# Performance work log

Hardware: AMD Instinct MI355X
Metric: run time of the kernel (lower is better)

## Reference

```python
import jax, jax.numpy as jnp
from jax import lax
import numpy as np

DIM = 8          # per-head dim
BN_EPS = 1e-5
ATT_EPS = 1e-15


def setup_inputs() -> dict:
    key = jax.random.key(0)
    ks = jax.random.split(key, 6)
    B, C, H, W = 2, 512, 128, 128
    total_dim = 512                      # heads(64) * dim(8)
    c3 = 3 * total_dim                   # 1536
    x = jax.random.normal(ks[0], (B, C, H, W), dtype=jnp.float32)
    w_qkv = jax.random.normal(ks[1], (c3, C), dtype=jnp.float32) * 0.02
    w_dw = jax.random.normal(ks[2], (c3, 1, 5, 5), dtype=jnp.float32) * 0.05
    w_pw = jax.random.normal(ks[3], (c3, 8, 1, 1), dtype=jnp.float32) * 0.1
    w_proj = jax.random.normal(ks[4], (512, 2 * total_dim), dtype=jnp.float32) * 0.02
    bn_gamma = jnp.ones((512,), jnp.float32)
    bn_beta = jnp.zeros((512,), jnp.float32)
    bn_mean = jnp.zeros((512,), jnp.float32)
    bn_var = jnp.ones((512,), jnp.float32)
    return {"x": x, "w_qkv": w_qkv, "w_dw": w_dw, "w_pw": w_pw, "w_proj": w_proj,
            "bn_gamma": bn_gamma, "bn_beta": bn_beta, "bn_mean": bn_mean, "bn_var": bn_var}


def reference(x, w_qkv, w_dw, w_pw, w_proj, bn_gamma, bn_beta, bn_mean, bn_var):
    B, C, H, W = x.shape
    dn = ('NCHW', 'OIHW', 'NCHW')
    # qkv: 1x1 conv, no bias/norm/act
    qkv = jnp.einsum('bchw,oc->bohw', x, w_qkv)  # (B, 1536, H, W)
    # multi-scale aggregation: 5x5 depthwise + 1x1 grouped (groups = 3*heads = 192)
    y = lax.conv_general_dilated(qkv, w_dw, (1, 1), [(2, 2), (2, 2)],
                                 feature_group_count=w_dw.shape[0], dimension_numbers=dn)
    y = lax.conv_general_dilated(y, w_pw, (1, 1), [(0, 0), (0, 0)],
                                 feature_group_count=w_pw.shape[0] // w_pw.shape[1],
                                 dimension_numbers=dn)
    mqkv = jnp.concatenate([qkv, y], axis=1)  # (B, 3072, H, W)
    N = H * W
    mqkv = mqkv.reshape(B, -1, 3 * DIM, N)    # (B, 128 heads, 24, N)
    q = jax.nn.relu(mqkv[:, :, :DIM])          # (B, h, d, N)
    k = jax.nn.relu(mqkv[:, :, DIM:2 * DIM])   # (B, h, d, N)
    v = mqkv[:, :, 2 * DIM:]                   # (B, h, d, N)
    v = jnp.pad(v, ((0, 0), (0, 0), (0, 1), (0, 0)), constant_values=1.0)  # (B,h,d+1,N)
    vk = jnp.einsum('bhdn,bhen->bhde', v, k)   # v @ k^T : (B,h,d+1,d)
    out = jnp.einsum('bhde,bhen->bhdn', vk, q)  # (B,h,d+1,N)
    out = out[:, :, :-1] / (out[:, :, -1:] + ATT_EPS)  # (B,h,d,N)
    out = out.reshape(B, -1, H, W)             # (B, 1024, H, W)
    # proj: 1x1 conv + bn2d (inference-mode affine), no act
    out = jnp.einsum('bchw,oc->bohw', out, w_proj)
    inv = bn_gamma / jnp.sqrt(bn_var + BN_EPS)
    out = out * inv[None, :, None, None] + (bn_beta - bn_mean * inv)[None, :, None, None]
    return out
```

## Files before the change

### kernel.cpp

```cpp
#include <hip/hip_runtime.h>

typedef __bf16 bf16_t;
typedef __bf16 bf16x8 __attribute__((ext_vector_type(8)));
typedef float  f32x4  __attribute__((ext_vector_type(4)));
typedef _Float16 h16;
typedef _Float16 h16x2 __attribute__((ext_vector_type(2)));
typedef _Float16 h16x4 __attribute__((ext_vector_type(4)));
typedef _Float16 h16x8 __attribute__((ext_vector_type(8)));

#define DEVINL __device__ __forceinline__

static constexpr size_t N_PIX = 16384;
static constexpr float  FIX_TAU = 2.5e-3f;

static constexpr size_t OFF_QB  = 0;
static constexpr size_t SZ_QB   = (size_t)512 * N_PIX * 2;
static constexpr size_t OFF_QR  = OFF_QB + SZ_QB;
static constexpr size_t SZ_QR   = SZ_QB;
static constexpr size_t OFF_KV  = OFF_QR + SZ_QR;
static constexpr size_t SZ_KV   = (size_t)1024 * N_PIX * 2;
static constexpr size_t OFF_Y   = OFF_KV + SZ_KV;
static constexpr size_t SZ_Y    = (size_t)1536 * N_PIX * 2;
static constexpr size_t OFF_ATT = OFF_Y + SZ_Y;
static constexpr size_t SZ_ATT  = (size_t)N_PIX * 1024 * 2;
static constexpr size_t OFF_XT  = OFF_ATT;
static constexpr size_t OFF_XTL = OFF_ATT + (size_t)N_PIX * 512 * 2;
static constexpr size_t OFF_WALL= OFF_ATT + SZ_ATT;
static constexpr size_t SZ_WALL = (size_t)1536 * 512 * 2;
static constexpr size_t OFF_WP  = OFF_WALL + SZ_WALL;
static constexpr size_t SZ_WP   = (size_t)512 * 1024 * 2;
static constexpr size_t OFF_VK  = OFF_WP + SZ_WP;
static constexpr size_t SZ_VK   = (size_t)128 * 72 * 4;
static constexpr size_t OFF_VKP = OFF_VK + SZ_VK;
static constexpr size_t SZ_VKP  = (size_t)128 * 8 * 72 * 4;
static constexpr size_t OFF_BNA = OFF_VKP + SZ_VKP;
static constexpr size_t OFF_ZP  = OFF_BNA + 2048;
static constexpr size_t OFF_W2  = OFF_ZP + 64;
static constexpr size_t SZ_W2   = (size_t)512 * 1024 * 2;
static constexpr size_t WS_NEEDED = OFF_W2 + SZ_W2;

DEVINL void gload16(const void* g, void* l) {
  __builtin_amdgcn_global_load_lds((const __attribute__((address_space(1))) void*)g,
                                   (__attribute__((address_space(3))) void*)l, 16, 0, 0);
}

__global__ __launch_bounds__(256)
void xpose_kernel(const float* __restrict__ x, h16* __restrict__ xT, h16* __restrict__ xTl) {
  __shared__ float t[32][33];
  const int n0 = blockIdx.x * 32, c0 = blockIdx.y * 32;
  const int tx = threadIdx.x & 31, ty = threadIdx.x >> 5;
#pragma unroll
  for (int r = 0; r < 4; ++r)
    t[ty + r * 8][tx] = x[(size_t)(c0 + ty + r * 8) * N_PIX + n0 + tx];
  __syncthreads();
  const int nl = threadIdx.x >> 3, sub = threadIdx.x & 7;
  const int c8 = (sub & 3) * 8, plane = sub >> 2;
  h16x8 o;
#pragma unroll
  for (int k = 0; k < 8; ++k) {
    const float v = t[c8 + k][nl];
    if (plane == 0) {
      o[k] = (h16)v;
    } else {
      const h16 hi = (h16)v;
      o[k] = (h16)(v - (float)hi);
    }
  }
  h16* dst = plane ? xTl : xT;
  *(h16x8*)&dst[(size_t)(n0 + nl) * 512 + c0 + c8] = o;
}

static constexpr int PREP_P1 = 1536 * 512;
static constexpr int PREP_P2 = 512 * 1024;
static constexpr int PREP_TOT = PREP_P1 + PREP_P2 + 512 + 16;
__global__ __launch_bounds__(256)
void prep_kernel(const float* __restrict__ wq, const float* __restrict__ wp,
                 const float* __restrict__ gam, const float* __restrict__ bet,
                 const float* __restrict__ mu, const float* __restrict__ va,
                 h16* __restrict__ wall, bf16_t* __restrict__ wpb,
                 float* __restrict__ bna, float* __restrict__ zp) {
  const int i = blockIdx.x * 256 + threadIdx.x;
  if (i < PREP_P1) {
    const int r = i >> 9, c = i & 511;
    int o;
    if (r < 512)       o = (r >> 3) * 24 + (r & 7);
    else if (r < 1024) o = ((r - 512) >> 3) * 24 + 8 + (r & 7);
    else               o = ((r - 1024) >> 3) * 24 + 16 + (r & 7);
    wall[i] = (h16)wq[(size_t)o * 512 + c];
  } else if (i < PREP_P1 + PREP_P2) {
    const int j = i - PREP_P1;
    const int m = j >> 10;
    const float inv = gam[m] / sqrtf(va[m] + 1e-5f);
    wpb[j] = (bf16_t)(wp[j] * inv);
  } else if (i < PREP_P1 + PREP_P2 + 512) {
    const int k = i - PREP_P1 - PREP_P2;
    const float inv = gam[k] / sqrtf(va[k] + 1e-5f);
    bna[k] = bet[k] - mu[k] * inv;
  } else if (i < PREP_TOT) {
    zp[i - (PREP_P1 + PREP_P2 + 512)] = 0.f;
  }
}

__global__ __launch_bounds__(256, 4)
void gemm_qkv_kernel(const h16* __restrict__ wall, const h16* __restrict__ xT,
                     h16* __restrict__ Qb, h16* __restrict__ Qr, h16* __restrict__ KV) {
  __shared__ __align__(16) h16 As[128 * 64];
  __shared__ __align__(16) h16 Bs[128 * 64];
  const int tid = threadIdx.x, wid = tid >> 6, lane = tid & 63;
  const int fr = lane & 15, fg = lane >> 4;
  const int wm = (wid >> 1) * 64, wn = (wid & 1) * 64;
  const int by = blockIdx.y;
  const bool isQ = by < 4;
  const int m0 = (isQ ? by : by - 4) * 128;
  const int n0 = blockIdx.x * 128;
  const h16* Aptr = wall + (size_t)by * 128 * 512;
  const int srow = tid >> 3;
  const int soff = (((tid & 7) ^ (srow & 7)) * 8);

  f32x4 acc[4][4] = {};

  for (int kk = 0; kk < 512; kk += 64) {
    __syncthreads();
#pragma unroll
    for (int r = 0; r < 4; ++r) {
      gload16(Aptr + (size_t)(srow + 32 * r) * 512 + kk + soff, As + (wid * 8 + 32 * r) * 64);
      gload16(xT + (size_t)(n0 + srow + 32 * r) * 512 + kk + soff, Bs + (wid * 8 + 32 * r) * 64);
    }
    __syncthreads();
#pragma unroll
    for (int ks = 0; ks < 2; ++ks) {
      h16x8 af[4], bfr[4];
#pragma unroll
      for (int i = 0; i < 4; ++i)
        af[i]  = *(const h16x8*)&As[(wm + i * 16 + fr) * 64 + (((ks * 4 + fg) ^ (fr & 7)) * 8)];
#pragma unroll
      for (int j = 0; j < 4; ++j)
        bfr[j] = *(const h16x8*)&Bs[(wn + j * 16 + fr) * 64 + (((ks * 4 + fg) ^ (fr & 7)) * 8)];
#pragma unroll
      for (int i = 0; i < 4; ++i)
#pragma unroll
        for (int j = 0; j < 4; ++j)
          acc[i][j] = __builtin_amdgcn_mfma_f32_16x16x32_f16(af[i], bfr[j], acc[i][j], 0, 0, 0);
    }
  }

#pragma unroll
  for (int i = 0; i < 4; ++i)
#pragma unroll
    for (int r = 0; r < 4; ++r) {
      const int m = m0 + wm + i * 16 + fg * 4 + r;
#pragma unroll
      for (int j = 0; j < 4; ++j) {
        const int n = n0 + wn + j * 16 + fr;
        const float v = acc[i][j][r];
        if (isQ) {
          Qb[(size_t)m * N_PIX + n] = (h16)v;
          Qr[(size_t)m * N_PIX + n] = (h16)fmaxf(0.f, v);
        } else {
          KV[(size_t)m * N_PIX + n] = (h16)v;
        }
      }
    }
}

__global__ __launch_bounds__(256)
void fix_kernel(const float* __restrict__ wq, const h16* __restrict__ xT,
                const h16* __restrict__ xTl, h16* __restrict__ Qr) {
  const int h = blockIdx.y;
  const int n = blockIdx.x * 256 + threadIdx.x;
  const int lane = threadIdx.x & 63;
  float mx = 0.f;
#pragma unroll
  for (int e = 0; e < 8; ++e)
    mx = fmaxf(mx, (float)Qr[(size_t)(h * 8 + e) * N_PIX + n]);
  unsigned long long mask = __ballot(mx < FIX_TAU);
  const int cb = blockIdx.x * 256 + ((int)threadIdx.x & ~63);
  while (mask) {
    const int bit = __builtin_ctzll(mask);
    mask &= mask - 1;
    const int np = cb + bit;
    const int c0 = lane * 8;
    const h16x8 xh = *(const h16x8*)&xT[(size_t)np * 512 + c0];
    const h16x8 xl = *(const h16x8*)&xTl[(size_t)np * 512 + c0];
    float xs[8];
#pragma unroll
    for (int u = 0; u < 8; ++u) xs[u] = (float)xh[u] + (float)xl[u];
    float acc[8];
#pragma unroll
    for (int e = 0; e < 8; ++e) {
      const float4 w0 = *(const float4*)&wq[(size_t)(h * 24 + e) * 512 + c0];
      const float4 w1 = *(const float4*)&wq[(size_t)(h * 24 + e) * 512 + c0 + 4];
      acc[e] = w0.x * xs[0] + w0.y * xs[1] + w0.z * xs[2] + w0.w * xs[3]
             + w1.x * xs[4] + w1.y * xs[5] + w1.z * xs[6] + w1.w * xs[7];
    }
#pragma unroll
    for (int e = 0; e < 8; ++e) {
      acc[e] += __shfl_xor(acc[e], 32); acc[e] += __shfl_xor(acc[e], 16);
      acc[e] += __shfl_xor(acc[e], 8);  acc[e] += __shfl_xor(acc[e], 4);
      acc[e] += __shfl_xor(acc[e], 2);  acc[e] += __shfl_xor(acc[e], 1);
    }
    if (lane < 8) {
      float v = acc[0];
#pragma unroll
      for (int e = 1; e < 8; ++e) if (lane == e) v = acc[e];
      Qr[(size_t)(h * 8 + lane) * N_PIX + np] = (h16)fmaxf(0.f, v);
    }
  }
}

__global__ __launch_bounds__(256, 4)
void gemm_proj_kernel(const bf16_t* __restrict__ A, const bf16_t* __restrict__ B,
                      float* __restrict__ Cout, const float* __restrict__ bna) {
  __shared__ __align__(16) bf16_t As[128 * 64];
  __shared__ __align__(16) bf16_t Bs[128 * 64];
  const int tid = threadIdx.x, wid = tid >> 6, lane = tid & 63;
  const int fr = lane & 15, fg = lane >> 4;
  const int wm = (wid >> 1) * 64, wn = (wid & 1) * 64;
  const int m0 = blockIdx.y * 128, n0 = blockIdx.x * 128;
  const int srow = tid >> 3;
  const int soff = (((tid & 7) ^ (srow & 7)) * 8);
  const bf16_t* Ab = A + (size_t)m0 * 1024;
  const bf16_t* Bb = B + (size_t)n0 * 1024;

  f32x4 acc[4][4] = {};

  for (int kk = 0; kk < 1024; kk += 64) {
    __syncthreads();
#pragma unroll
    for (int r = 0; r < 4; ++r) {
      gload16(Ab + (size_t)(srow + 32 * r) * 1024 + kk + soff, As + (wid * 8 + 32 * r) * 64);
      gload16(Bb + (size_t)(srow + 32 * r) * 1024 + kk + soff, Bs + (wid * 8 + 32 * r) * 64);
    }
    __syncthreads();
#pragma unroll
    for (int ks = 0; ks < 2; ++ks) {
      bf16x8 af[4], bfr[4];
#pragma unroll
      for (int i = 0; i < 4; ++i)
        af[i]  = *(const bf16x8*)&As[(wm + i * 16 + fr) * 64 + (((ks * 4 + fg) ^ (fr & 7)) * 8)];
#pragma unroll
      for (int j = 0; j < 4; ++j)
        bfr[j] = *(const bf16x8*)&Bs[(wn + j * 16 + fr) * 64 + (((ks * 4 + fg) ^ (fr & 7)) * 8)];
#pragma unroll
      for (int i = 0; i < 4; ++i)
#pragma unroll
        for (int j = 0; j < 4; ++j)
          acc[i][j] = __builtin_amdgcn_mfma_f32_16x16x32_bf16(af[i], bfr[j], acc[i][j], 0, 0, 0);
    }
  }

#pragma unroll
  for (int i = 0; i < 4; ++i)
#pragma unroll
    for (int r = 0; r < 4; ++r) {
      const int m = m0 + wm + i * 16 + fg * 4 + r;
      const float sh = bna[m];
#pragma unroll
      for (int j = 0; j < 4; ++j)
        Cout[(size_t)m * N_PIX + n0 + wn + j * 16 + fr] = acc[i][j][r] + sh;
    }
}

__global__ __launch_bounds__(256)
void dwpw_kernel(const h16* __restrict__ Qb, const h16* __restrict__ KV,
                 const float* __restrict__ wdw, const float* __restrict__ wpw,
                 const h16* __restrict__ zp, h16* __restrict__ y) {
  const int g = blockIdx.y, t = blockIdx.x;
  const int typ = g % 3, head = g / 3;
  const int ty0 = (t >> 1) * 16, tx0 = (t & 1) * 64;
  const int tid = threadIdx.x, wid = tid >> 6, lane = tid & 63;
  __shared__ __align__(16) h16 sin_[8][20][80];
  __shared__ h16x2 swd2[8][25];
  __shared__ h16x2 swp2[8][8];
  if (tid < 200) {
    const h16 w = (h16)wdw[(g * 8 + tid / 25) * 25 + tid % 25];
    h16x2 w2; w2[0] = w; w2[1] = w;
    swd2[tid / 25][tid % 25] = w2;
  }
  if (tid < 64) {
    const h16 w = (h16)wpw[(g * 8 + (tid >> 3)) * 8 + (tid & 7)];
    h16x2 w2; w2[0] = w; w2[1] = w;
    swp2[tid >> 3][tid & 7] = w2;
  }
  const h16* plane = (typ == 0) ? (Qb + (size_t)head * 8 * N_PIX)
                                : (KV + (size_t)((typ == 2 ? 512 : 0) + head * 8) * N_PIX);
  h16* sflat = &sin_[0][0][0];
  for (int base = wid * 64; base < 1600; base += 256) {
    const int id  = base + lane;
    const int ch  = id / 200;
    const int rem = id - ch * 200;
    const int row = rem / 10;
    const int c6  = rem - row * 10;
    const int gy  = ty0 + row - 2;
    const int gx  = tx0 + c6 * 8 - 8;
    const bool ok = ((unsigned)gy < 128u) && ((unsigned)gx < 128u);
    const h16* src = ok ? (plane + (size_t)ch * N_PIX + gy * 128 + gx) : zp;
    gload16(src, sflat + (size_t)base * 8);
  }
  __syncthreads();

  const int px4 = (tid & 15) * 4, py = tid >> 4;
  h16x2 dwa[8][2];
#pragma unroll
  for (int ch = 0; ch < 8; ++ch) {
    h16x2 A0 = 0, A1 = 0;
#pragma unroll
    for (int di = 0; di < 5; ++di) {
      const uint2 w0 = *(const uint2*)&sin_[ch][py + di][px4 + 4];
      const uint2 w1 = *(const uint2*)&sin_[ch][py + di][px4 + 8];
      const uint2 w2v = *(const uint2*)&sin_[ch][py + di][px4 + 12];
      const unsigned u1 = w0.y, u2 = w1.x, u3 = w1.y, u4 = w2v.x;
      const h16x2 P2 = __builtin_bit_cast(h16x2, u1);
      const h16x2 P3 = __builtin_bit_cast(h16x2, (u2 << 16) | (u1 >> 16));
      const h16x2 P4 = __builtin_bit_cast(h16x2, u2);
      const h16x2 P5 = __builtin_bit_cast(h16x2, (u3 << 16) | (u2 >> 16));
      const h16x2 P6 = __builtin_bit_cast(h16x2, u3);
      const h16x2 P7 = __builtin_bit_cast(h16x2, (u4 << 16) | (u3 >> 16));
      const h16x2 P8 = __builtin_bit_cast(h16x2, u4);
      h16x2 wd;
      wd = swd2[ch][di * 5 + 0]; A0 += wd * P2; A1 += wd * P4;
      wd = swd2[ch][di * 5 + 1]; A0 += wd * P3; A1 += wd * P5;
      wd = swd2[ch][di * 5 + 2]; A0 += wd * P4; A1 += wd * P6;
      wd = swd2[ch][di * 5 + 3]; A0 += wd * P5; A1 += wd * P7;
      wd = swd2[ch][di * 5 + 4]; A0 += wd * P6; A1 += wd * P8;
    }
    dwa[ch][0] = A0; dwa[ch][1] = A1;
  }
#pragma unroll
  for (int oc = 0; oc < 8; ++oc) {
    h16x2 o0 = 0, o1 = 0;
#pragma unroll
    for (int ic = 0; ic < 8; ++ic) {
      const h16x2 w = swp2[oc][ic];
      o0 += w * dwa[ic][0];
      o1 += w * dwa[ic][1];
    }
    h16x4 ov; ov[0] = o0[0]; ov[1] = o0[1]; ov[2] = o1[0]; ov[3] = o1[1];
    *(h16x4*)&y[(size_t)(8 * g + oc) * N_PIX + (ty0 + py) * 128 + tx0 + px4] = ov;
  }
}

__global__ __launch_bounds__(256)
void vk_partial_kernel(const h16* __restrict__ KV, const h16* __restrict__ yb,
                       float* __restrict__ part) {
  const int h = blockIdx.y, s = blockIdx.x;
  const h16 *kb, *vb;
  if (h < 64) {
    kb = KV + (size_t)(h * 8) * N_PIX;
    vb = KV + (size_t)(512 + h * 8) * N_PIX;
  } else {
    kb = yb + (size_t)(24 * (h - 64) + 8) * N_PIX;
    vb = yb + (size_t)(24 * (h - 64) + 16) * N_PIX;
  }
  float a[8][8] = {};
  float ak[8] = {};
  const int p0 = s * 2048 + (int)threadIdx.x * 8;
  float kq[8][8], vq[8][8];
#pragma unroll
  for (int e = 0; e < 8; ++e) {
    h16x8 kk = *(const h16x8*)&kb[(size_t)e * N_PIX + p0];
#pragma unroll
    for (int u = 0; u < 8; ++u) kq[e][u] = fmaxf(0.f, (float)kk[u]);
  }
#pragma unroll
  for (int d = 0; d < 8; ++d) {
    h16x8 vv = *(const h16x8*)&vb[(size_t)d * N_PIX + p0];
#pragma unroll
    for (int u = 0; u < 8; ++u) vq[d][u] = (float)vv[u];
  }
#pragma unroll
  for (int d = 0; d < 8; ++d)
#pragma unroll
    for (int e = 0; e < 8; ++e)
#pragma unroll
      for (int u = 0; u < 8; ++u) a[d][e] += vq[d][u] * kq[e][u];
#pragma unroll
  for (int e = 0; e < 8; ++e)
#pragma unroll
    for (int u = 0; u < 8; ++u) ak[e] += kq[e][u];

  __shared__ float red[4][72];
  const int lane = threadIdx.x & 63, wid = threadIdx.x >> 6;
#pragma unroll
  for (int i = 0; i < 72; ++i) {
    float v = (i < 64) ? a[i >> 3][i & 7] : ak[i - 64];
    v += __shfl_xor(v, 32); v += __shfl_xor(v, 16); v += __shfl_xor(v, 8);
    v += __shfl_xor(v, 4);  v += __shfl_xor(v, 2);  v += __shfl_xor(v, 1);
    if (lane == 0) red[wid][i] = v;
  }
  __syncthreads();
  if (threadIdx.x < 72) {
    const float sum_ = red[0][threadIdx.x] + red[1][threadIdx.x] + red[2][threadIdx.x] + red[3][threadIdx.x];
    part[((size_t)h * 8 + s) * 72 + threadIdx.x] = sum_;
  }
}

__global__ __launch_bounds__(128)
void vk_reduce_kernel(const float* __restrict__ part, float* __restrict__ vk) {
  const int h = blockIdx.x;
  const int i = threadIdx.x;
  if (i < 72) {
    float s = 0.f;
#pragma unroll
    for (int t = 0; t < 8; ++t) s += part[((size_t)h * 8 + t) * 72 + i];
    vk[(size_t)h * 72 + i] = s;
  }
}

__global__ __launch_bounds__(256)
void w2_kernel(const bf16_t* __restrict__ wpb, const float* __restrict__ vkm,
               bf16_t* __restrict__ W2) {
  const int idx = blockIdx.x * 256 + threadIdx.x;
  const int m = idx >> 10, c = idx & 1023;
  const int h = c >> 3, e = c & 7;
  float s = 0.f;
#pragma unroll
  for (int d = 0; d < 8; ++d)
    s += (float)wpb[(size_t)m * 1024 + h * 8 + d] * vkm[h * 72 + d * 8 + e];
  W2[idx] = (bf16_t)s;
}

__global__ __launch_bounds__(256)
void qn_kernel(const h16* __restrict__ Qr, const h16* __restrict__ yb,
               const float* __restrict__ vk, bf16_t* __restrict__ qnT) {
  const int n0 = blockIdx.x * 32;
  const int tid = threadIdx.x;
  const int px = tid & 31, hl = tid >> 5;
  __shared__ __align__(16) bf16_t att_s[32 * 512];
  __shared__ float ak_s[64];
  for (int grp = 0; grp < 2; ++grp) {
    for (int hg = 0; hg < 8; ++hg) {
      __syncthreads();
      if (tid < 64)
        ak_s[tid] = vk[((size_t)grp * 64 + hg * 8 + (tid >> 3)) * 72 + 64 + (tid & 7)];
      __syncthreads();
      const int hh = hg * 8 + hl;
      float q[8];
      if (grp == 0) {
        const h16* plane = Qr + (size_t)(hh * 8) * N_PIX + n0 + px;
#pragma unroll
        for (int e = 0; e < 8; ++e) q[e] = (float)plane[(size_t)e * N_PIX];
      } else {
        const h16* plane = yb + (size_t)(24 * hh) * N_PIX + n0 + px;
#pragma unroll
        for (int e = 0; e < 8; ++e) q[e] = fmaxf(0.f, (float)plane[(size_t)e * N_PIX]);
      }
      float den = 1e-15f;
#pragma unroll
      for (int e = 0; e < 8; ++e) den += ak_s[hl * 8 + e] * q[e];
      const float rden = 1.0f / den;
      bf16x8 r8;
#pragma unroll
      for (int e = 0; e < 8; ++e) r8[e] = (bf16_t)(q[e] * rden);
      const int chunk = hg * 8 + hl;
      *(bf16x8*)&att_s[px * 512 + ((chunk ^ (px & 7)) << 3)] = r8;
    }
    __syncthreads();
    bf16_t* dst = qnT + (size_t)n0 * 1024 + grp * 512;
    for (int i = tid; i < 2048; i += 256) {
      const int r = i >> 6, cc = i & 63;
      bf16x8 v = *(const bf16x8*)&att_s[r * 512 + (((cc ^ (r & 7))) << 3)];
      *(bf16x8*)&dst[(size_t)r * 1024 + cc * 8] = v;
    }
  }
}

extern "C" void kernel_launch(void* const* d_in, const int* in_sizes, int n_in,
                              void* d_out, int out_size, void* d_ws, size_t ws_size,
                              hipStream_t stream) {
  if (ws_size < WS_NEEDED) return;
  const float* x      = (const float*)d_in[0];
  const float* w_qkv  = (const float*)d_in[1];
  const float* w_dw   = (const float*)d_in[2];
  const float* w_pw   = (const float*)d_in[3];
  const float* w_proj = (const float*)d_in[4];
  const float* gam    = (const float*)d_in[5];
  const float* bet    = (const float*)d_in[6];
  const float* mu     = (const float*)d_in[7];
  const float* va     = (const float*)d_in[8];

  char* w = (char*)d_ws;
  h16*    Qb   = (h16*)(w + OFF_QB);
  h16*    Qr   = (h16*)(w + OFF_QR);
  h16*    KV   = (h16*)(w + OFF_KV);
  h16*    yb   = (h16*)(w + OFF_Y);
  h16*    xT   = (h16*)(w + OFF_XT);
  h16*    xTl  = (h16*)(w + OFF_XTL);
  bf16_t* qnT  = (bf16_t*)(w + OFF_ATT);
  h16*    wall = (h16*)(w + OFF_WALL);
  bf16_t* wpb  = (bf16_t*)(w + OFF_WP);
  bf16_t* W2   = (bf16_t*)(w + OFF_W2);
  float*  vk   = (float*)(w + OFF_VK);
  float*  part = (float*)(w + OFF_VKP);
  float*  bna  = (float*)(w + OFF_BNA);
  float*  zp   = (float*)(w + OFF_ZP);

  dim3 blk(256);
  prep_kernel<<<dim3((PREP_TOT + 255) / 256), blk, 0, stream>>>(
      w_qkv, w_proj, gam, bet, mu, va, wall, wpb, bna, zp);

  for (int b = 0; b < 2; ++b) {
    const float* xb = x + (size_t)b * 512 * N_PIX;
    float* outb = (float*)d_out + (size_t)b * 512 * N_PIX;
    xpose_kernel<<<dim3(512, 16), blk, 0, stream>>>(xb, xT, xTl);
    gemm_qkv_kernel<<<dim3(128, 12), blk, 0, stream>>>(wall, xT, Qb, Qr, KV);
    fix_kernel<<<dim3(64, 64), blk, 0, stream>>>(w_qkv, xT, xTl, Qr);
    dwpw_kernel<<<dim3(16, 192), blk, 0, stream>>>(Qb, KV, w_dw, w_pw, (const h16*)zp, yb);
    vk_partial_kernel<<<dim3(8, 128), blk, 0, stream>>>(KV, yb, part);
    vk_reduce_kernel<<<dim3(128), dim3(128), 0, stream>>>(part, vk);
    w2_kernel<<<dim3(512 * 1024 / 256), blk, 0, stream>>>(wpb, vk, W2);
    qn_kernel<<<dim3(512), blk, 0, stream>>>(Qr, yb, vk, qnT);
    gemm_proj_kernel<<<dim3(128, 4), blk, 0, stream>>>(W2, qnT, outb, bna);
  }
}
```

Baseline: 354.9 us.

## Widen GEMM N tiles to 256 and move ReLU-Q write into fix kernel

Both the QKV and projection GEMMs now use a 128x256 block tile, with each wave computing 64x128. This halves the grid and improves reuse of the A tile, at the cost of more accumulator registers and lower occupancy (launch bounds drop from 4 to 2 blocks per CU). The QKV GEMM no longer writes the ReLU'd Q copy. Instead the fix kernel reads Qb, applies ReLU, and writes Qr for non-flagged pixels, which removes one large store from the GEMM epilogue.

```diff
diff --git a/kernel.cpp b/kernel.cpp
--- a/kernel.cpp
+++ b/kernel.cpp
@@ -101,45 +101,52 @@
   }
 }
 
-__global__ __launch_bounds__(256, 4)
+__global__ __launch_bounds__(256, 2)
 void gemm_qkv_kernel(const h16* __restrict__ wall, const h16* __restrict__ xT,
-                     h16* __restrict__ Qb, h16* __restrict__ Qr, h16* __restrict__ KV) {
+                     h16* __restrict__ Qb, h16* __restrict__ KV) {
   __shared__ __align__(16) h16 As[128 * 64];
-  __shared__ __align__(16) h16 Bs[128 * 64];
+  __shared__ __align__(16) h16 Bs[256 * 64];
   const int tid = threadIdx.x, wid = tid >> 6, lane = tid & 63;
   const int fr = lane & 15, fg = lane >> 4;
-  const int wm = (wid >> 1) * 64, wn = (wid & 1) * 64;
+  const int wm = (wid >> 1) * 64, wn = (wid & 1) * 128;
   const int by = blockIdx.y;
   const bool isQ = by < 4;
   const int m0 = (isQ ? by : by - 4) * 128;
-  const int n0 = blockIdx.x * 128;
+  const int n0 = blockIdx.x * 256;
   const h16* Aptr = wall + (size_t)by * 128 * 512;
-  const int srow = tid >> 3;
-  const int soff = (((tid & 7) ^ (srow & 7)) * 8);
-
-  f32x4 acc[4][4] = {};
+
+  f32x4 acc[4][8] = {};
 
   for (int kk = 0; kk < 512; kk += 64) {
     __syncthreads();
 #pragma unroll
     for (int r = 0; r < 4; ++r) {
-      gload16(Aptr + (size_t)(srow + 32 * r) * 512 + kk + soff, As + (wid * 8 + 32 * r) * 64);
-      gload16(xT + (size_t)(n0 + srow + 32 * r) * 512 + kk + soff, Bs + (wid * 8 + 32 * r) * 64);
+      const int c = wid * 64 + lane + 256 * r;
+      const int row = c >> 3, cc = c & 7;
+      gload16(Aptr + (size_t)row * 512 + kk + ((cc ^ (row & 7)) * 8),
+              As + (size_t)(wid * 64 + 256 * r) * 8);
+    }
+#pragma unroll
+    for (int r = 0; r < 8; ++r) {
+      const int c = wid * 64 + lane + 256 * r;
+      const int row = c >> 3, cc = c & 7;
+      gload16(xT + (size_t)(n0 + row) * 512 + kk + ((cc ^ (row & 7)) * 8),
+              Bs + (size_t)(wid * 64 + 256 * r) * 8);
     }
     __syncthreads();
 #pragma unroll
     for (int ks = 0; ks < 2; ++ks) {
-      h16x8 af[4], bfr[4];
+      h16x8 af[4], bfr[8];
 #pragma unroll
       for (int i = 0; i < 4; ++i)
         af[i]  = *(const h16x8*)&As[(wm + i * 16 + fr) * 64 + (((ks * 4 + fg) ^ (fr & 7)) * 8)];
 #pragma unroll
-      for (int j = 0; j < 4; ++j)
+      for (int j = 0; j < 8; ++j)
         bfr[j] = *(const h16x8*)&Bs[(wn + j * 16 + fr) * 64 + (((ks * 4 + fg) ^ (fr & 7)) * 8)];
 #pragma unroll
       for (int i = 0; i < 4; ++i)
 #pragma unroll
-        for (int j = 0; j < 4; ++j)
+        for (int j = 0; j < 8; ++j)
           acc[i][j] = __builtin_amdgcn_mfma_f32_16x16x32_f16(af[i], bfr[j], acc[i][j], 0, 0, 0);
     }
   }
@@ -149,31 +156,36 @@
 #pragma unroll
     for (int r = 0; r < 4; ++r) {
       const int m = m0 + wm + i * 16 + fg * 4 + r;
-#pragma unroll
-      for (int j = 0; j < 4; ++j) {
+      h16* dst = isQ ? Qb : KV;
+#pragma unroll
+      for (int j = 0; j < 8; ++j) {
         const int n = n0 + wn + j * 16 + fr;
-        const float v = acc[i][j][r];
-        if (isQ) {
-          Qb[(size_t)m * N_PIX + n] = (h16)v;
-          Qr[(size_t)m * N_PIX + n] = (h16)fmaxf(0.f, v);
-        } else {
-          KV[(size_t)m * N_PIX + n] = (h16)v;
-        }
+        dst[(size_t)m * N_PIX + n] = (h16)acc[i][j][r];
       }
     }
 }
 
 __global__ __launch_bounds__(256)
 void fix_kernel(const float* __restrict__ wq, const h16* __restrict__ xT,
-                const h16* __restrict__ xTl, h16* __restrict__ Qr) {
+                const h16* __restrict__ xTl, const h16* __restrict__ Qb,
+                h16* __restrict__ Qr) {
   const int h = blockIdx.y;
   const int n = blockIdx.x * 256 + threadIdx.x;
   const int lane = threadIdx.x & 63;
+  float q[8];
   float mx = 0.f;
 #pragma unroll
-  for (int e = 0; e < 8; ++e)
-    mx = fmaxf(mx, (float)Qr[(size_t)(h * 8 + e) * N_PIX + n]);
-  unsigned long long mask = __ballot(mx < FIX_TAU);
+  for (int e = 0; e < 8; ++e) {
+    q[e] = fmaxf(0.f, (float)Qb[(size_t)(h * 8 + e) * N_PIX + n]);
+    mx = fmaxf(mx, q[e]);
+  }
+  const bool flag = mx < FIX_TAU;
+  if (!flag) {
+#pragma unroll
+    for (int e = 0; e < 8; ++e)
+      Qr[(size_t)(h * 8 + e) * N_PIX + n] = (h16)q[e];
+  }
+  unsigned long long mask = __ballot(flag);
   const int cb = blockIdx.x * 256 + ((int)threadIdx.x & ~63);
   while (mask) {
     const int bit = __builtin_ctzll(mask);
@@ -208,43 +220,49 @@
   }
 }
 
-__global__ __launch_bounds__(256, 4)
+__global__ __launch_bounds__(256, 2)
 void gemm_proj_kernel(const bf16_t* __restrict__ A, const bf16_t* __restrict__ B,
                       float* __restrict__ Cout, const float* __restrict__ bna) {
   __shared__ __align__(16) bf16_t As[128 * 64];
-  __shared__ __align__(16) bf16_t Bs[128 * 64];
+  __shared__ __align__(16) bf16_t Bs[256 * 64];
   const int tid = threadIdx.x, wid = tid >> 6, lane = tid & 63;
   const int fr = lane & 15, fg = lane >> 4;
-  const int wm = (wid >> 1) * 64, wn = (wid & 1) * 64;
-  const int m0 = blockIdx.y * 128, n0 = blockIdx.x * 128;
-  const int srow = tid >> 3;
-  const int soff = (((tid & 7) ^ (srow & 7)) * 8);
+  const int wm = (wid >> 1) * 64, wn = (wid & 1) * 128;
+  const int m0 = blockIdx.y * 128, n0 = blockIdx.x * 256;
   const bf16_t* Ab = A + (size_t)m0 * 1024;
-  const bf16_t* Bb = B + (size_t)n0 * 1024;
-
-  f32x4 acc[4][4] = {};
+
+  f32x4 acc[4][8] = {};
 
   for (int kk = 0; kk < 1024; kk += 64) {
     __syncthreads();
 #pragma unroll
     for (int r = 0; r < 4; ++r) {
-      gload16(Ab + (size_t)(srow + 32 * r) * 1024 + kk + soff, As + (wid * 8 + 32 * r) * 64);
-      gload16(Bb + (size_t)(srow + 32 * r) * 1024 + kk + soff, Bs + (wid * 8 + 32 * r) * 64);
+      const int c = wid * 64 + lane + 256 * r;
+      const int row = c >> 3, cc = c & 7;
+      gload16(Ab + (size_t)row * 1024 + kk + ((cc ^ (row & 7)) * 8),
+              As + (size_t)(wid * 64 + 256 * r) * 8);
+    }
+#pragma unroll
+    for (int r = 0; r < 8; ++r) {
+      const int c = wid * 64 + lane + 256 * r;
+      const int row = c >> 3, cc = c & 7;
+      gload16(B + (size_t)(n0 + row) * 1024 + kk + ((cc ^ (row & 7)) * 8),
+              Bs + (size_t)(wid * 64 + 256 * r) * 8);
     }
     __syncthreads();
 #pragma unroll
     for (int ks = 0; ks < 2; ++ks) {
-      bf16x8 af[4], bfr[4];
+      bf16x8 af[4], bfr[8];
 #pragma unroll
       for (int i = 0; i < 4; ++i)
         af[i]  = *(const bf16x8*)&As[(wm + i * 16 + fr) * 64 + (((ks * 4 + fg) ^ (fr & 7)) * 8)];
 #pragma unroll
-      for (int j = 0; j < 4; ++j)
+      for (int j = 0; j < 8; ++j)
         bfr[j] = *(const bf16x8*)&Bs[(wn + j * 16 + fr) * 64 + (((ks * 4 + fg) ^ (fr & 7)) * 8)];
 #pragma unroll
       for (int i = 0; i < 4; ++i)
 #pragma unroll
-        for (int j = 0; j < 4; ++j)
+        for (int j = 0; j < 8; ++j)
           acc[i][j] = __builtin_amdgcn_mfma_f32_16x16x32_bf16(af[i], bfr[j], acc[i][j], 0, 0, 0);
     }
   }
@@ -256,7 +274,7 @@
       const int m = m0 + wm + i * 16 + fg * 4 + r;
       const float sh = bna[m];
 #pragma unroll
-      for (int j = 0; j < 4; ++j)
+      for (int j = 0; j < 8; ++j)
         Cout[(size_t)m * N_PIX + n0 + wn + j * 16 + fr] = acc[i][j][r] + sh;
     }
 }
@@ -503,13 +521,13 @@
     const float* xb = x + (size_t)b * 512 * N_PIX;
     float* outb = (float*)d_out + (size_t)b * 512 * N_PIX;
     xpose_kernel<<<dim3(512, 16), blk, 0, stream>>>(xb, xT, xTl);
-    gemm_qkv_kernel<<<dim3(128, 12), blk, 0, stream>>>(wall, xT, Qb, Qr, KV);
-    fix_kernel<<<dim3(64, 64), blk, 0, stream>>>(w_qkv, xT, xTl, Qr);
+    gemm_qkv_kernel<<<dim3(64, 12), blk, 0, stream>>>(wall, xT, Qb, KV);
+    fix_kernel<<<dim3(64, 64), blk, 0, stream>>>(w_qkv, xT, xTl, Qb, Qr);
     dwpw_kernel<<<dim3(16, 192), blk, 0, stream>>>(Qb, KV, w_dw, w_pw, (const h16*)zp, yb);
     vk_partial_kernel<<<dim3(8, 128), blk, 0, stream>>>(KV, yb, part);
     vk_reduce_kernel<<<dim3(128), dim3(128), 0, stream>>>(part, vk);
     w2_kernel<<<dim3(512 * 1024 / 256), blk, 0, stream>>>(wpb, vk, W2);
     qn_kernel<<<dim3(512), blk, 0, stream>>>(Qr, yb, vk, qnT);
-    gemm_proj_kernel<<<dim3(128, 4), blk, 0, stream>>>(W2, qnT, outb, bna);
-  }
-}
+    gemm_proj_kernel<<<dim3(64, 4), blk, 0, stream>>>(W2, qnT, outb, bna);
+  }
+}
```

After: 362.3 us. 2.1% more time.

## Drop separate ReLU Q buffer and widen QKV GEMM tile to 128x256

Applied to the files above, without the earlier changes.

The QKV GEMM no longer writes a second ReLU'd copy of Q. The precision-fix kernel patches the raw Q buffer in place, and the qn kernel applies ReLU when it loads Q. This removes one full-size fp16 store stream and its buffer. The GEMM block tile also grows from 128x128 to 128x256 with twice the accumulators per wave. That halves the grid and improves operand reuse, but raises register and LDS pressure and lowers the occupancy target to 2.

```diff
diff --git a/kernel.cpp b/kernel.cpp
--- a/kernel.cpp
+++ b/kernel.cpp
@@ -15,9 +15,7 @@
 
 static constexpr size_t OFF_QB  = 0;
 static constexpr size_t SZ_QB   = (size_t)512 * N_PIX * 2;
-static constexpr size_t OFF_QR  = OFF_QB + SZ_QB;
-static constexpr size_t SZ_QR   = SZ_QB;
-static constexpr size_t OFF_KV  = OFF_QR + SZ_QR;
+static constexpr size_t OFF_KV  = OFF_QB + SZ_QB;
 static constexpr size_t SZ_KV   = (size_t)1024 * N_PIX * 2;
 static constexpr size_t OFF_Y   = OFF_KV + SZ_KV;
 static constexpr size_t SZ_Y    = (size_t)1536 * N_PIX * 2;
@@ -101,45 +99,52 @@
   }
 }
 
-__global__ __launch_bounds__(256, 4)
+__global__ __launch_bounds__(256, 2)
 void gemm_qkv_kernel(const h16* __restrict__ wall, const h16* __restrict__ xT,
-                     h16* __restrict__ Qb, h16* __restrict__ Qr, h16* __restrict__ KV) {
+                     h16* __restrict__ Qb, h16* __restrict__ KV) {
   __shared__ __align__(16) h16 As[128 * 64];
-  __shared__ __align__(16) h16 Bs[128 * 64];
+  __shared__ __align__(16) h16 Bs[256 * 64];
   const int tid = threadIdx.x, wid = tid >> 6, lane = tid & 63;
   const int fr = lane & 15, fg = lane >> 4;
-  const int wm = (wid >> 1) * 64, wn = (wid & 1) * 64;
+  const int wm = (wid >> 1) * 64, wn = (wid & 1) * 128;
   const int by = blockIdx.y;
   const bool isQ = by < 4;
   const int m0 = (isQ ? by : by - 4) * 128;
-  const int n0 = blockIdx.x * 128;
+  const int n0 = blockIdx.x * 256;
   const h16* Aptr = wall + (size_t)by * 128 * 512;
-  const int srow = tid >> 3;
-  const int soff = (((tid & 7) ^ (srow & 7)) * 8);
-
-  f32x4 acc[4][4] = {};
+
+  f32x4 acc[4][8] = {};
 
   for (int kk = 0; kk < 512; kk += 64) {
     __syncthreads();
 #pragma unroll
     for (int r = 0; r < 4; ++r) {
-      gload16(Aptr + (size_t)(srow + 32 * r) * 512 + kk + soff, As + (wid * 8 + 32 * r) * 64);
-      gload16(xT + (size_t)(n0 + srow + 32 * r) * 512 + kk + soff, Bs + (wid * 8 + 32 * r) * 64);
+      const int c = wid * 64 + lane + 256 * r;
+      const int row = c >> 3, cc = c & 7;
+      gload16(Aptr + (size_t)row * 512 + kk + ((cc ^ (row & 7)) * 8),
+              As + (size_t)(wid * 64 + 256 * r) * 8);
+    }
+#pragma unroll
+    for (int r = 0; r < 8; ++r) {
+      const int c = wid * 64 + lane + 256 * r;
+      const int row = c >> 3, cc = c & 7;
+      gload16(xT + (size_t)(n0 + row) * 512 + kk + ((cc ^ (row & 7)) * 8),
+              Bs + (size_t)(wid * 64 + 256 * r) * 8);
     }
     __syncthreads();
 #pragma unroll
     for (int ks = 0; ks < 2; ++ks) {
-      h16x8 af[4], bfr[4];
+      h16x8 af[4], bfr[8];
 #pragma unroll
       for (int i = 0; i < 4; ++i)
         af[i]  = *(const h16x8*)&As[(wm + i * 16 + fr) * 64 + (((ks * 4 + fg) ^ (fr & 7)) * 8)];
 #pragma unroll
-      for (int j = 0; j < 4; ++j)
+      for (int j = 0; j < 8; ++j)
         bfr[j] = *(const h16x8*)&Bs[(wn + j * 16 + fr) * 64 + (((ks * 4 + fg) ^ (fr & 7)) * 8)];
 #pragma unroll
       for (int i = 0; i < 4; ++i)
 #pragma unroll
-        for (int j = 0; j < 4; ++j)
+        for (int j = 0; j < 8; ++j)
           acc[i][j] = __builtin_amdgcn_mfma_f32_16x16x32_f16(af[i], bfr[j], acc[i][j], 0, 0, 0);
     }
   }
@@ -149,30 +154,25 @@
 #pragma unroll
     for (int r = 0; r < 4; ++r) {
       const int m = m0 + wm + i * 16 + fg * 4 + r;
-#pragma unroll
-      for (int j = 0; j < 4; ++j) {
+      h16* dst = isQ ? Qb : KV;
+#pragma unroll
+      for (int j = 0; j < 8; ++j) {
         const int n = n0 + wn + j * 16 + fr;
-        const float v = acc[i][j][r];
-        if (isQ) {
-          Qb[(size_t)m * N_PIX + n] = (h16)v;
-          Qr[(size_t)m * N_PIX + n] = (h16)fmaxf(0.f, v);
-        } else {
-          KV[(size_t)m * N_PIX + n] = (h16)v;
-        }
+        dst[(size_t)m * N_PIX + n] = (h16)acc[i][j][r];
       }
     }
 }
 
 __global__ __launch_bounds__(256)
 void fix_kernel(const float* __restrict__ wq, const h16* __restrict__ xT,
-                const h16* __restrict__ xTl, h16* __restrict__ Qr) {
+                const h16* __restrict__ xTl, h16* __restrict__ Qb) {
   const int h = blockIdx.y;
   const int n = blockIdx.x * 256 + threadIdx.x;
   const int lane = threadIdx.x & 63;
   float mx = 0.f;
 #pragma unroll
   for (int e = 0; e < 8; ++e)
-    mx = fmaxf(mx, (float)Qr[(size_t)(h * 8 + e) * N_PIX + n]);
+    mx = fmaxf(mx, (float)Qb[(size_t)(h * 8 + e) * N_PIX + n]);
   unsigned long long mask = __ballot(mx < FIX_TAU);
   const int cb = blockIdx.x * 256 + ((int)threadIdx.x & ~63);
   while (mask) {
@@ -203,7 +203,7 @@
       float v = acc[0];
 #pragma unroll
       for (int e = 1; e < 8; ++e) if (lane == e) v = acc[e];
-      Qr[(size_t)(h * 8 + lane) * N_PIX + np] = (h16)fmaxf(0.f, v);
+      Qb[(size_t)(h * 8 + lane) * N_PIX + np] = (h16)v;
     }
   }
 }
@@ -421,7 +421,7 @@
 }
 
 __global__ __launch_bounds__(256)
-void qn_kernel(const h16* __restrict__ Qr, const h16* __restrict__ yb,
+void qn_kernel(const h16* __restrict__ Qb, const h16* __restrict__ yb,
                const float* __restrict__ vk, bf16_t* __restrict__ qnT) {
   const int n0 = blockIdx.x * 32;
   const int tid = threadIdx.x;
@@ -437,9 +437,9 @@
       const int hh = hg * 8 + hl;
       float q[8];
       if (grp == 0) {
-        const h16* plane = Qr + (size_t)(hh * 8) * N_PIX + n0 + px;
-#pragma unroll
-        for (int e = 0; e < 8; ++e) q[e] = (float)plane[(size_t)e * N_PIX];
+        const h16* plane = Qb + (size_t)(hh * 8) * N_PIX + n0 + px;
+#pragma unroll
+        for (int e = 0; e < 8; ++e) q[e] = fmaxf(0.f, (float)plane[(size_t)e * N_PIX]);
       } else {
         const h16* plane = yb + (size_t)(24 * hh) * N_PIX + n0 + px;
 #pragma unroll
@@ -481,7 +481,6 @@
 
   char* w = (char*)d_ws;
   h16*    Qb   = (h16*)(w + OFF_QB);
-  h16*    Qr   = (h16*)(w + OFF_QR);
   h16*    KV   = (h16*)(w + OFF_KV);
   h16*    yb   = (h16*)(w + OFF_Y);
   h16*    xT   = (h16*)(w + OFF_XT);
@@ -503,13 +502,13 @@
     const float* xb = x + (size_t)b * 512 * N_PIX;
     float* outb = (float*)d_out + (size_t)b * 512 * N_PIX;
     xpose_kernel<<<dim3(512, 16), blk, 0, stream>>>(xb, xT, xTl);
-    gemm_qkv_kernel<<<dim3(128, 12), blk, 0, stream>>>(wall, xT, Qb, Qr, KV);
-    fix_kernel<<<dim3(64, 64), blk, 0, stream>>>(w_qkv, xT, xTl, Qr);
+    gemm_qkv_kernel<<<dim3(64, 12), blk, 0, stream>>>(wall, xT, Qb, KV);
+    fix_kernel<<<dim3(64, 64), blk, 0, stream>>>(w_qkv, xT, xTl, Qb);
     dwpw_kernel<<<dim3(16, 192), blk, 0, stream>>>(Qb, KV, w_dw, w_pw, (const h16*)zp, yb);
     vk_partial_kernel<<<dim3(8, 128), blk, 0, stream>>>(KV, yb, part);
     vk_reduce_kernel<<<dim3(128), dim3(128), 0, stream>>>(part, vk);
     w2_kernel<<<dim3(512 * 1024 / 256), blk, 0, stream>>>(wpb, vk, W2);
-    qn_kernel<<<dim3(512), blk, 0, stream>>>(Qr, yb, vk, qnT);
+    qn_kernel<<<dim3(512), blk, 0, stream>>>(Qb, yb, vk, qnT);
     gemm_proj_kernel<<<dim3(128, 4), blk, 0, stream>>>(W2, qnT, outb, bna);
   }
 }
```

Measured after the change: 344.9 us. 1.03x faster.
